# Performance work log

Measured on AMD Instinct MI355X. Metric: run time of the kernel, lower is better.

The kernel has to match this reference:

```python
import jax, jax.numpy as jnp
import numpy as np

N, A, B, H = 16, 2048, 2048, 64


def setup_inputs() -> dict:
    key = jax.random.key(0)
    k1, k2, k3, k4 = jax.random.split(key, 4)
    query = jax.random.normal(k1, (N, A, H), dtype=jnp.float32)
    key_t = jax.random.normal(k2, (N, B, H), dtype=jnp.float32)
    value = jax.random.normal(k3, (N, B, H), dtype=jnp.float32)
    mask = jax.random.randint(k4, (N, B), 0, 2).astype(bool)  # True = masked out
    return {"query": query, "key": key_t, "value": value, "mask": mask}


def reference(query, key, value, mask):
    # attention_product: scaled dot product -> (n, a, b) logits
    h = query.shape[-1]
    scale = 1.0 / jnp.sqrt(jnp.asarray(h, dtype=query.dtype))
    logit = jnp.einsum("nah,nbh->nab", query, key) * scale
    # mask (n, b) broadcast over query axis; masked positions -> -inf
    logit = jnp.where(mask[:, None, :], -jnp.inf, logit)
    attn = jax.nn.softmax(logit, axis=-1)
    # dropout_rate = 0.0 (eval) -> identity
    context = jnp.einsum("nab,nbh->nah", attn, value)
    return context
```

## Files before the change

kernel.cpp:

```cpp
#include <hip/hip_runtime.h>

#define NB 16
#define AQ 2048
#define BKV 2048
#define HD 64

#define QSCALE 0.18033688f
#define MBIAS -43000.0f
#define DTHR 8.0f

typedef float f32x4 __attribute__((ext_vector_type(4)));
typedef float f32x16 __attribute__((ext_vector_type(16)));
typedef short bf16x8 __attribute__((ext_vector_type(8)));
typedef int int4v __attribute__((ext_vector_type(4)));

__device__ __forceinline__ short f2bf(float f) {
  return __builtin_bit_cast(short, static_cast<__bf16>(f));
}
__device__ __forceinline__ unsigned pk2(float a, float b) {
  unsigned lo = (unsigned short)f2bf(a);
  unsigned hh = (unsigned short)f2bf(b);
  return lo | (hh << 16);
}

__global__ __launch_bounds__(256) void prepack(const float* __restrict__ K,
                                               const float* __restrict__ V,
                                               const int* __restrict__ M,
                                               short* __restrict__ Kb,
                                               short* __restrict__ Vt,
                                               unsigned* __restrict__ Mb) {
  if (blockIdx.x < 1024) {
    size_t base = ((size_t)blockIdx.x * 256 + threadIdx.x) * 8;
    f32x4 a = *(const f32x4*)(K + base);
    f32x4 b = *(const f32x4*)(K + base + 4);
    bf16x8 o;
#pragma unroll
    for (int i = 0; i < 4; ++i) {
      o[i] = f2bf(a[i]);
      o[i + 4] = f2bf(b[i]);
    }
    *(bf16x8*)(Kb + base) = o;
  } else if (blockIdx.x < 1536) {
    unsigned vb = blockIdx.x - 1024;
    int n = vb >> 5;
    int b0 = (vb & 31) * 64;
    int t = threadIdx.x;
    __shared__ short tile[64][68];
    int rb = t >> 4;
    int hc = (t & 15) * 4;
#pragma unroll
    for (int j = 0; j < 4; ++j) {
      int r = rb + 16 * j;
      f32x4 v = *(const f32x4*)(V + ((size_t)n * BKV + b0 + r) * HD + hc);
#pragma unroll
      for (int i = 0; i < 4; ++i) tile[r][hc + i] = f2bf(v[i]);
    }
    __syncthreads();
    int hr = t >> 2;
    int bb = (t & 3) * 16;
    bf16x8 o0, o1;
#pragma unroll
    for (int j = 0; j < 8; ++j) {
      o0[j] = tile[bb + j][hr];
      o1[j] = tile[bb + 8 + j][hr];
    }
    short* dst = Vt + ((size_t)n * HD + hr) * BKV + b0 + bb;
    *(bf16x8*)dst = o0;
    *(bf16x8*)(dst + 8) = o1;
  } else {
    unsigned gw = (blockIdx.x - 1536) * 256 + threadIdx.x;
    int n = (int)(gw >> 6);
    int ww = (int)(gw & 63u);
    const int* src = M + (size_t)n * BKV + ww * 32;
    unsigned bits = 0;
#pragma unroll
    for (int j = 0; j < 32; ++j) bits |= (src[j] ? 1u : 0u) << j;
    Mb[n * 64 + ww] = bits;
  }
}

template <int PRE>
__global__ __launch_bounds__(256, 3) void attn_fwd(
    const float* __restrict__ Q, const float* __restrict__ K,
    const float* __restrict__ V, const int* __restrict__ M,
    const short* __restrict__ Kb, const short* __restrict__ Vt,
    const unsigned* __restrict__ Mb, float* __restrict__ O) {
  unsigned orig = blockIdx.x;
  unsigned wg = (orig & 7u) * 128u + (orig >> 3);
  int n = (int)(wg >> 6);
  int q0 = (int)(wg & 63u) * 32;

  int w = threadIdx.x >> 6;
  int lane = threadIdx.x & 63;
  int hi = lane >> 5;
  int li = lane & 31;

  const float* Qn = Q + (size_t)n * AQ * HD;
  const float* Kn = K + (size_t)n * BKV * HD;
  const float* Vn = V + (size_t)n * BKV * HD;
  const short* Kbn = Kb + (size_t)n * BKV * HD;
  const short* Vtn = Vt + (size_t)n * HD * BKV;
  const unsigned* Mbn = Mb + (size_t)n * 64;
  const int* Mn = M + (size_t)n * BKV;

  __shared__ __align__(16) float pacc[4][32][68];
  __shared__ float Ml[4][2][32];

  bf16x8 qb[4];
#pragma unroll
  for (int ks = 0; ks < 4; ++ks) {
    const float* qp = Qn + (size_t)(q0 + li) * HD + 16 * ks + 8 * hi;
    f32x4 a = *(const f32x4*)qp;
    f32x4 b = *(const f32x4*)(qp + 4);
#pragma unroll
    for (int i = 0; i < 4; ++i) {
      qb[ks][i] = f2bf(a[i] * QSCALE);
      qb[ks][i + 4] = f2bf(b[i] * QSCALE);
    }
  }

  f32x16 acc0 = {};
  f32x16 acc1 = {};
  float m_run = -1e30f;
  float l_run = 0.f;

  const int bstart = w * (BKV / 4);

  auto LOADK = [&](int b0, bf16x8(&ka)[4]) {
#pragma unroll
    for (int ks = 0; ks < 4; ++ks) {
      if constexpr (PRE) {
        ka[ks] = *(const bf16x8*)(Kbn + (size_t)(b0 + li) * HD + 16 * ks + 8 * hi);
      } else {
        const float* kp = Kn + (size_t)(b0 + li) * HD + 16 * ks + 8 * hi;
        f32x4 k0 = *(const f32x4*)kp;
        f32x4 k1 = *(const f32x4*)(kp + 4);
#pragma unroll
        for (int i = 0; i < 4; ++i) {
          ka[ks][i] = f2bf(k0[i]);
          ka[ks][i + 4] = f2bf(k1[i]);
        }
      }
    }
  };
  auto LOADMB = [&](int b0) -> unsigned {
    if constexpr (PRE) return Mbn[b0 >> 5];
    return 0u;
  };

  auto TILE = [&](int b0, const bf16x8(&ka)[4], unsigned mb) {
    bf16x8 va0, va1, va2, va3;
    if constexpr (PRE) {
      const short* vp0 = Vtn + (size_t)li * BKV + b0 + 8 * hi;
      const short* vp1 = Vtn + (size_t)(32 + li) * BKV + b0 + 8 * hi;
      va0 = *(const bf16x8*)vp0;
      va1 = *(const bf16x8*)(vp0 + 16);
      va2 = *(const bf16x8*)vp1;
      va3 = *(const bf16x8*)(vp1 + 16);
    } else {
#pragma unroll
      for (int j = 0; j < 8; ++j) {
        va0[j] = f2bf(Vn[(size_t)(b0 + 8 * hi + j) * HD + li]);
        va1[j] = f2bf(Vn[(size_t)(b0 + 16 + 8 * hi + j) * HD + li]);
        va2[j] = f2bf(Vn[(size_t)(b0 + 8 * hi + j) * HD + 32 + li]);
        va3[j] = f2bf(Vn[(size_t)(b0 + 16 + 8 * hi + j) * HD + 32 + li]);
      }
    }

    f32x16 st;
    if constexpr (PRE) {
      unsigned ub = mb >> (4 * hi);
#pragma unroll
      for (int r = 0; r < 16; ++r) {
        int pos = (r & 3) + 8 * (r >> 2);
        st[r] = ((ub >> pos) & 1u) ? MBIAS : 0.f;
      }
    } else {
      int4v mv[4];
#pragma unroll
      for (int j = 0; j < 4; ++j) mv[j] = *(const int4v*)(Mn + b0 + 8 * j + 4 * hi);
#pragma unroll
      for (int j = 0; j < 4; ++j)
#pragma unroll
        for (int r = 0; r < 4; ++r) st[4 * j + r] = mv[j][r] ? MBIAS : 0.f;
    }

#pragma unroll
    for (int ks = 0; ks < 4; ++ks)
      st = __builtin_amdgcn_mfma_f32_32x32x16_bf16(ka[ks], qb[ks], st, 0, 0, 0);

    float a0 = fmaxf(fmaxf(st[0], st[1]), st[2]);
    float a1 = fmaxf(fmaxf(st[3], st[4]), st[5]);
    float a2 = fmaxf(fmaxf(st[6], st[7]), st[8]);
    float a3 = fmaxf(fmaxf(st[9], st[10]), st[11]);
    float a4 = fmaxf(fmaxf(st[12], st[13]), st[14]);
    float mt = fmaxf(fmaxf(fmaxf(a0, a1), fmaxf(a2, a3)), fmaxf(a4, st[15]));
    mt = fmaxf(mt, __shfl_xor(mt, 32));

    if (!__all(mt - m_run <= DTHR)) {
      float m_new = fmaxf(m_run, mt);
      float fac = exp2f(m_run - m_new);
      l_run *= fac;
#pragma unroll
      for (int i = 0; i < 16; ++i) {
        acc0[i] *= fac;
        acc1[i] *= fac;
      }
      m_run = m_new;
    }

#pragma unroll
    for (int i = 0; i < 16; ++i) st[i] = exp2f(st[i] - m_run);
    float s0 = (st[0] + st[1]) + (st[2] + st[3]);
    float s1 = (st[4] + st[5]) + (st[6] + st[7]);
    float s2 = (st[8] + st[9]) + (st[10] + st[11]);
    float s3 = (st[12] + st[13]) + (st[14] + st[15]);
    float rs = (s0 + s1) + (s2 + s3);
    rs += __shfl_xor(rs, 32);
    l_run += rs;

    unsigned w8[8];
#pragma unroll
    for (int j = 0; j < 8; ++j) w8[j] = pk2(st[2 * j], st[2 * j + 1]);
    auto s02 = __builtin_amdgcn_permlane32_swap((int)w8[0], (int)w8[2], false, false);
    auto s13 = __builtin_amdgcn_permlane32_swap((int)w8[1], (int)w8[3], false, false);
    auto s46 = __builtin_amdgcn_permlane32_swap((int)w8[4], (int)w8[6], false, false);
    auto s57 = __builtin_amdgcn_permlane32_swap((int)w8[5], (int)w8[7], false, false);
    int4v p0 = {static_cast<int>(s02[0]), static_cast<int>(s13[0]),
                static_cast<int>(s02[1]), static_cast<int>(s13[1])};
    int4v p1 = {static_cast<int>(s46[0]), static_cast<int>(s57[0]),
                static_cast<int>(s46[1]), static_cast<int>(s57[1])};
    bf16x8 pb0 = __builtin_bit_cast(bf16x8, p0);
    bf16x8 pb1 = __builtin_bit_cast(bf16x8, p1);

    acc0 = __builtin_amdgcn_mfma_f32_32x32x16_bf16(va0, pb0, acc0, 0, 0, 0);
    acc0 = __builtin_amdgcn_mfma_f32_32x32x16_bf16(va1, pb1, acc0, 0, 0, 0);
    acc1 = __builtin_amdgcn_mfma_f32_32x32x16_bf16(va2, pb0, acc1, 0, 0, 0);
    acc1 = __builtin_amdgcn_mfma_f32_32x32x16_bf16(va3, pb1, acc1, 0, 0, 0);
  };

  bf16x8 kaA[4], kaB[4];
  LOADK(bstart, kaA);
  unsigned mbA = LOADMB(bstart), mbB;
#pragma unroll 1
  for (int t = 0; t < 16; t += 2) {
    const int b0 = bstart + t * 32;
    LOADK(b0 + 32, kaB);
    mbB = LOADMB(b0 + 32);
    TILE(b0, kaA, mbA);
    if (t < 14) {
      LOADK(b0 + 64, kaA);
      mbA = LOADMB(b0 + 64);
    }
    TILE(b0 + 32, kaB, mbB);
  }

  if (hi == 0) {
    Ml[w][0][li] = m_run;
    Ml[w][1][li] = l_run;
  }
#pragma unroll
  for (int reg = 0; reg < 16; ++reg) {
    int hrow = (reg & 3) + 8 * (reg >> 2) + 4 * hi;
    pacc[w][li][hrow] = acc0[reg];
    pacc[w][li][32 + hrow] = acc1[reg];
  }
  __syncthreads();

  {
    int tid = threadIdx.x;
    int q = tid >> 3;
    int hb = (tid & 7) * 8;
    float m0 = Ml[0][0][q], m1 = Ml[1][0][q];
    float m2 = Ml[2][0][q], m3 = Ml[3][0][q];
    float mmax = fmaxf(fmaxf(m0, m1), fmaxf(m2, m3));
    float f[4] = {exp2f(m0 - mmax), exp2f(m1 - mmax), exp2f(m2 - mmax),
                  exp2f(m3 - mmax)};
    float l = f[0] * Ml[0][1][q] + f[1] * Ml[1][1][q] + f[2] * Ml[2][1][q] +
              f[3] * Ml[3][1][q];
    float inv = 1.0f / l;
    float* op = O + ((size_t)n * AQ + q0 + q) * HD + hb;
#pragma unroll
    for (int t = 0; t < 2; ++t) {
      f32x4 o = {0.f, 0.f, 0.f, 0.f};
#pragma unroll
      for (int ww = 0; ww < 4; ++ww) {
        f32x4 a = *(const f32x4*)&pacc[ww][q][hb + 4 * t];
#pragma unroll
        for (int i = 0; i < 4; ++i) o[i] += f[ww] * a[i];
      }
      f32x4 res;
#pragma unroll
      for (int i = 0; i < 4; ++i) res[i] = o[i] * inv;
      *(f32x4*)(op + 4 * t) = res;
    }
  }
}

extern "C" void kernel_launch(void* const* d_in, const int* in_sizes, int n_in,
                              void* d_out, int out_size, void* d_ws, size_t ws_size,
                              hipStream_t stream) {
  const float* q = (const float*)d_in[0];
  const float* k = (const float*)d_in[1];
  const float* v = (const float*)d_in[2];
  const int* m = (const int*)d_in[3];
  float* o = (float*)d_out;

  const size_t kv_elems = (size_t)NB * BKV * HD;
  const size_t mb_words = (size_t)NB * 64;
  const size_t need = kv_elems * 2 * sizeof(short) + mb_words * 4;

  if (ws_size >= need) {
    short* kb = (short*)d_ws;
    short* vt = kb + kv_elems;
    unsigned* mb = (unsigned*)(vt + kv_elems);
    prepack<<<dim3(1540), dim3(256), 0, stream>>>(k, v, m, kb, vt, mb);
    attn_fwd<1><<<dim3(NB * (AQ / 32)), dim3(256), 0, stream>>>(q, k, v, m, kb, vt, mb, o);
  } else {
    attn_fwd<0><<<dim3(NB * (AQ / 32)), dim3(256), 0, stream>>>(q, k, v, m, nullptr, nullptr, nullptr, o);
  }
}
```

Before: 140.9 us.

## Drop prepack kernel and convert K/V/mask to bf16 inline in attention

Removes the separate prepack kernel that converted K to bf16, transposed V to bf16 and bit-packed the mask into workspace. The attention kernel now always reads fp32 K, V and the int mask directly and converts them per tile. This saves a kernel launch and the extra write/read round trip through workspace. In exchange each block loads twice the bytes for K and V, uses strided scalar V loads, and repeats the conversion work across the 64 query blocks per batch.

```diff
diff --git a/kernel.cpp b/kernel.cpp
--- a/kernel.cpp
+++ b/kernel.cpp
@@ -23,68 +23,10 @@
   return lo | (hh << 16);
 }
 
-__global__ __launch_bounds__(256) void prepack(const float* __restrict__ K,
-                                               const float* __restrict__ V,
-                                               const int* __restrict__ M,
-                                               short* __restrict__ Kb,
-                                               short* __restrict__ Vt,
-                                               unsigned* __restrict__ Mb) {
-  if (blockIdx.x < 1024) {
-    size_t base = ((size_t)blockIdx.x * 256 + threadIdx.x) * 8;
-    f32x4 a = *(const f32x4*)(K + base);
-    f32x4 b = *(const f32x4*)(K + base + 4);
-    bf16x8 o;
-#pragma unroll
-    for (int i = 0; i < 4; ++i) {
-      o[i] = f2bf(a[i]);
-      o[i + 4] = f2bf(b[i]);
-    }
-    *(bf16x8*)(Kb + base) = o;
-  } else if (blockIdx.x < 1536) {
-    unsigned vb = blockIdx.x - 1024;
-    int n = vb >> 5;
-    int b0 = (vb & 31) * 64;
-    int t = threadIdx.x;
-    __shared__ short tile[64][68];
-    int rb = t >> 4;
-    int hc = (t & 15) * 4;
-#pragma unroll
-    for (int j = 0; j < 4; ++j) {
-      int r = rb + 16 * j;
-      f32x4 v = *(const f32x4*)(V + ((size_t)n * BKV + b0 + r) * HD + hc);
-#pragma unroll
-      for (int i = 0; i < 4; ++i) tile[r][hc + i] = f2bf(v[i]);
-    }
-    __syncthreads();
-    int hr = t >> 2;
-    int bb = (t & 3) * 16;
-    bf16x8 o0, o1;
-#pragma unroll
-    for (int j = 0; j < 8; ++j) {
-      o0[j] = tile[bb + j][hr];
-      o1[j] = tile[bb + 8 + j][hr];
-    }
-    short* dst = Vt + ((size_t)n * HD + hr) * BKV + b0 + bb;
-    *(bf16x8*)dst = o0;
-    *(bf16x8*)(dst + 8) = o1;
-  } else {
-    unsigned gw = (blockIdx.x - 1536) * 256 + threadIdx.x;
-    int n = (int)(gw >> 6);
-    int ww = (int)(gw & 63u);
-    const int* src = M + (size_t)n * BKV + ww * 32;
-    unsigned bits = 0;
-#pragma unroll
-    for (int j = 0; j < 32; ++j) bits |= (src[j] ? 1u : 0u) << j;
-    Mb[n * 64 + ww] = bits;
-  }
-}
-
-template <int PRE>
 __global__ __launch_bounds__(256, 3) void attn_fwd(
     const float* __restrict__ Q, const float* __restrict__ K,
     const float* __restrict__ V, const int* __restrict__ M,
-    const short* __restrict__ Kb, const short* __restrict__ Vt,
-    const unsigned* __restrict__ Mb, float* __restrict__ O) {
+    float* __restrict__ O) {
   unsigned orig = blockIdx.x;
   unsigned wg = (orig & 7u) * 128u + (orig >> 3);
   int n = (int)(wg >> 6);
@@ -98,9 +40,6 @@
   const float* Qn = Q + (size_t)n * AQ * HD;
   const float* Kn = K + (size_t)n * BKV * HD;
   const float* Vn = V + (size_t)n * BKV * HD;
-  const short* Kbn = Kb + (size_t)n * BKV * HD;
-  const short* Vtn = Vt + (size_t)n * HD * BKV;
-  const unsigned* Mbn = Mb + (size_t)n * 64;
   const int* Mn = M + (size_t)n * BKV;
 
   __shared__ __align__(16) float pacc[4][32][68];
@@ -129,61 +68,37 @@
   auto LOADK = [&](int b0, bf16x8(&ka)[4]) {
 #pragma unroll
     for (int ks = 0; ks < 4; ++ks) {
-      if constexpr (PRE) {
-        ka[ks] = *(const bf16x8*)(Kbn + (size_t)(b0 + li) * HD + 16 * ks + 8 * hi);
-      } else {
-        const float* kp = Kn + (size_t)(b0 + li) * HD + 16 * ks + 8 * hi;
-        f32x4 k0 = *(const f32x4*)kp;
-        f32x4 k1 = *(const f32x4*)(kp + 4);
-#pragma unroll
-        for (int i = 0; i < 4; ++i) {
-          ka[ks][i] = f2bf(k0[i]);
-          ka[ks][i + 4] = f2bf(k1[i]);
-        }
+      const float* kp = Kn + (size_t)(b0 + li) * HD + 16 * ks + 8 * hi;
+      f32x4 k0 = *(const f32x4*)kp;
+      f32x4 k1 = *(const f32x4*)(kp + 4);
+#pragma unroll
+      for (int i = 0; i < 4; ++i) {
+        ka[ks][i] = f2bf(k0[i]);
+        ka[ks][i + 4] = f2bf(k1[i]);
       }
     }
   };
-  auto LOADMB = [&](int b0) -> unsigned {
-    if constexpr (PRE) return Mbn[b0 >> 5];
-    return 0u;
-  };
-
-  auto TILE = [&](int b0, const bf16x8(&ka)[4], unsigned mb) {
+
+  auto TILE = [&](int b0, const bf16x8(&ka)[4]) {
     bf16x8 va0, va1, va2, va3;
-    if constexpr (PRE) {
-      const short* vp0 = Vtn + (size_t)li * BKV + b0 + 8 * hi;
-      const short* vp1 = Vtn + (size_t)(32 + li) * BKV + b0 + 8 * hi;
-      va0 = *(const bf16x8*)vp0;
-      va1 = *(const bf16x8*)(vp0 + 16);
-      va2 = *(const bf16x8*)vp1;
-      va3 = *(const bf16x8*)(vp1 + 16);
-    } else {
-#pragma unroll
-      for (int j = 0; j < 8; ++j) {
-        va0[j] = f2bf(Vn[(size_t)(b0 + 8 * hi + j) * HD + li]);
-        va1[j] = f2bf(Vn[(size_t)(b0 + 16 + 8 * hi + j) * HD + li]);
-        va2[j] = f2bf(Vn[(size_t)(b0 + 8 * hi + j) * HD + 32 + li]);
-        va3[j] = f2bf(Vn[(size_t)(b0 + 16 + 8 * hi + j) * HD + 32 + li]);
-      }
-    }
-
+#pragma unroll
+    for (int j = 0; j < 8; ++j) {
+      const float* vr0 = Vn + (size_t)(b0 + 8 * hi + j) * HD;
+      const float* vr1 = Vn + (size_t)(b0 + 16 + 8 * hi + j) * HD;
+      va0[j] = f2bf(vr0[li]);
+      va2[j] = f2bf(vr0[32 + li]);
+      va1[j] = f2bf(vr1[li]);
+      va3[j] = f2bf(vr1[32 + li]);
+    }
+
+    int4v mv[4];
+#pragma unroll
+    for (int j = 0; j < 4; ++j) mv[j] = *(const int4v*)(Mn + b0 + 8 * j + 4 * hi);
     f32x16 st;
-    if constexpr (PRE) {
-      unsigned ub = mb >> (4 * hi);
-#pragma unroll
-      for (int r = 0; r < 16; ++r) {
-        int pos = (r & 3) + 8 * (r >> 2);
-        st[r] = ((ub >> pos) & 1u) ? MBIAS : 0.f;
-      }
-    } else {
-      int4v mv[4];
-#pragma unroll
-      for (int j = 0; j < 4; ++j) mv[j] = *(const int4v*)(Mn + b0 + 8 * j + 4 * hi);
-#pragma unroll
-      for (int j = 0; j < 4; ++j)
-#pragma unroll
-        for (int r = 0; r < 4; ++r) st[4 * j + r] = mv[j][r] ? MBIAS : 0.f;
-    }
+#pragma unroll
+    for (int j = 0; j < 4; ++j)
+#pragma unroll
+      for (int r = 0; r < 4; ++r) st[4 * j + r] = mv[j][r] ? MBIAS : 0.f;
 
 #pragma unroll
     for (int ks = 0; ks < 4; ++ks)
@@ -241,18 +156,13 @@
 
   bf16x8 kaA[4], kaB[4];
   LOADK(bstart, kaA);
-  unsigned mbA = LOADMB(bstart), mbB;
 #pragma unroll 1
   for (int t = 0; t < 16; t += 2) {
     const int b0 = bstart + t * 32;
     LOADK(b0 + 32, kaB);
-    mbB = LOADMB(b0 + 32);
-    TILE(b0, kaA, mbA);
-    if (t < 14) {
-      LOADK(b0 + 64, kaA);
-      mbA = LOADMB(b0 + 64);
-    }
-    TILE(b0 + 32, kaB, mbB);
+    TILE(b0, kaA);
+    if (t < 14) LOADK(b0 + 64, kaA);
+    TILE(b0 + 32, kaB);
   }
 
   if (hi == 0) {
@@ -305,18 +215,5 @@
   const float* v = (const float*)d_in[2];
   const int* m = (const int*)d_in[3];
   float* o = (float*)d_out;
-
-  const size_t kv_elems = (size_t)NB * BKV * HD;
-  const size_t mb_words = (size_t)NB * 64;
-  const size_t need = kv_elems * 2 * sizeof(short) + mb_words * 4;
-
-  if (ws_size >= need) {
-    short* kb = (short*)d_ws;
-    short* vt = kb + kv_elems;
-    unsigned* mb = (unsigned*)(vt + kv_elems);
-    prepack<<<dim3(1540), dim3(256), 0, stream>>>(k, v, m, kb, vt, mb);
-    attn_fwd<1><<<dim3(NB * (AQ / 32)), dim3(256), 0, stream>>>(q, k, v, m, kb, vt, mb, o);
-  } else {
-    attn_fwd<0><<<dim3(NB * (AQ / 32)), dim3(256), 0, stream>>>(q, k, v, m, nullptr, nullptr, nullptr, o);
-  }
-}
+  attn_fwd<<<dim3(NB * (AQ / 32)), dim3(256), 0, stream>>>(q, k, v, m, o);
+}
```

New measurement: 161.1 us. 1.14x slower.

## Software-pipeline QK and softmax-PV stages across tiles, use permlane32 reductions

Applied to the files above, without the earlier changes.

Splits the per-tile body into QK, softmax+PV, and V-load stages and schedules the next tile's QK MFMAs before the current tile's softmax. The aim is to overlap matrix-core work with the exp/max ALU work and to prefetch V one tile ahead. Cross-half reductions now use permlane32_swap instead of __shfl_xor, which avoids LDS-based shuffles. The cost is more live registers (two score tiles plus K and V buffers), which may lower occupancy or cause spills.

```diff
diff --git a/kernel.cpp b/kernel.cpp
--- a/kernel.cpp
+++ b/kernel.cpp
@@ -21,6 +21,18 @@
   unsigned lo = (unsigned short)f2bf(a);
   unsigned hh = (unsigned short)f2bf(b);
   return lo | (hh << 16);
+}
+__device__ __forceinline__ float xmax32(float x) {
+  int xi = __builtin_bit_cast(int, x);
+  auto p = __builtin_amdgcn_permlane32_swap(xi, xi, false, false);
+  return fmaxf(__builtin_bit_cast(float, (int)p[0]),
+               __builtin_bit_cast(float, (int)p[1]));
+}
+__device__ __forceinline__ float xadd32(float x) {
+  int xi = __builtin_bit_cast(int, x);
+  auto p = __builtin_amdgcn_permlane32_swap(xi, xi, false, false);
+  return __builtin_bit_cast(float, (int)p[0]) +
+         __builtin_bit_cast(float, (int)p[1]);
 }
 
 __global__ __launch_bounds__(256) void prepack(const float* __restrict__ K,
@@ -147,9 +159,7 @@
     if constexpr (PRE) return Mbn[b0 >> 5];
     return 0u;
   };
-
-  auto TILE = [&](int b0, const bf16x8(&ka)[4], unsigned mb) {
-    bf16x8 va0, va1, va2, va3;
+  auto LOADV = [&](int b0, bf16x8& va0, bf16x8& va1, bf16x8& va2, bf16x8& va3) {
     if constexpr (PRE) {
       const short* vp0 = Vtn + (size_t)li * BKV + b0 + 8 * hi;
       const short* vp1 = Vtn + (size_t)(32 + li) * BKV + b0 + 8 * hi;
@@ -160,13 +170,17 @@
     } else {
 #pragma unroll
       for (int j = 0; j < 8; ++j) {
-        va0[j] = f2bf(Vn[(size_t)(b0 + 8 * hi + j) * HD + li]);
-        va1[j] = f2bf(Vn[(size_t)(b0 + 16 + 8 * hi + j) * HD + li]);
-        va2[j] = f2bf(Vn[(size_t)(b0 + 8 * hi + j) * HD + 32 + li]);
-        va3[j] = f2bf(Vn[(size_t)(b0 + 16 + 8 * hi + j) * HD + 32 + li]);
-      }
-    }
-
+        const float* vr0 = Vn + (size_t)(b0 + 8 * hi + j) * HD;
+        const float* vr1 = Vn + (size_t)(b0 + 16 + 8 * hi + j) * HD;
+        va0[j] = f2bf(vr0[li]);
+        va2[j] = f2bf(vr0[32 + li]);
+        va1[j] = f2bf(vr1[li]);
+        va3[j] = f2bf(vr1[32 + li]);
+      }
+    }
+  };
+
+  auto QK = [&](int b0, const bf16x8(&ka)[4], unsigned mb) -> f32x16 {
     f32x16 st;
     if constexpr (PRE) {
       unsigned ub = mb >> (4 * hi);
@@ -184,18 +198,21 @@
 #pragma unroll
         for (int r = 0; r < 4; ++r) st[4 * j + r] = mv[j][r] ? MBIAS : 0.f;
     }
-
 #pragma unroll
     for (int ks = 0; ks < 4; ++ks)
       st = __builtin_amdgcn_mfma_f32_32x32x16_bf16(ka[ks], qb[ks], st, 0, 0, 0);
-
+    return st;
+  };
+
+  auto SMPV = [&](f32x16& st, const bf16x8& va0, const bf16x8& va1,
+                  const bf16x8& va2, const bf16x8& va3) {
     float a0 = fmaxf(fmaxf(st[0], st[1]), st[2]);
     float a1 = fmaxf(fmaxf(st[3], st[4]), st[5]);
     float a2 = fmaxf(fmaxf(st[6], st[7]), st[8]);
     float a3 = fmaxf(fmaxf(st[9], st[10]), st[11]);
     float a4 = fmaxf(fmaxf(st[12], st[13]), st[14]);
     float mt = fmaxf(fmaxf(fmaxf(a0, a1), fmaxf(a2, a3)), fmaxf(a4, st[15]));
-    mt = fmaxf(mt, __shfl_xor(mt, 32));
+    mt = xmax32(mt);
 
     if (!__all(mt - m_run <= DTHR)) {
       float m_new = fmaxf(m_run, mt);
@@ -215,9 +232,7 @@
     float s1 = (st[4] + st[5]) + (st[6] + st[7]);
     float s2 = (st[8] + st[9]) + (st[10] + st[11]);
     float s3 = (st[12] + st[13]) + (st[14] + st[15]);
-    float rs = (s0 + s1) + (s2 + s3);
-    rs += __shfl_xor(rs, 32);
-    l_run += rs;
+    l_run += xadd32((s0 + s1) + (s2 + s3));
 
     unsigned w8[8];
 #pragma unroll
@@ -239,20 +254,33 @@
     acc1 = __builtin_amdgcn_mfma_f32_32x32x16_bf16(va3, pb1, acc1, 0, 0, 0);
   };
 
-  bf16x8 kaA[4], kaB[4];
-  LOADK(bstart, kaA);
-  unsigned mbA = LOADMB(bstart), mbB;
+  bf16x8 ka0[4], ka1[4];
+  bf16x8 va0, va1, va2, va3;
+  LOADK(bstart, ka0);
+  unsigned mb0 = LOADMB(bstart);
+  LOADK(bstart + 32, ka1);
+  unsigned mb1 = LOADMB(bstart + 32);
+  LOADV(bstart, va0, va1, va2, va3);
+  f32x16 stA = QK(bstart, ka0, mb0);
+  f32x16 stB;
+
 #pragma unroll 1
   for (int t = 0; t < 16; t += 2) {
     const int b0 = bstart + t * 32;
-    LOADK(b0 + 32, kaB);
-    mbB = LOADMB(b0 + 32);
-    TILE(b0, kaA, mbA);
-    if (t < 14) {
-      LOADK(b0 + 64, kaA);
-      mbA = LOADMB(b0 + 64);
-    }
-    TILE(b0 + 32, kaB, mbB);
+    if (t + 2 < 16) {
+      LOADK(b0 + 64, ka0);
+      mb0 = LOADMB(b0 + 64);
+    }
+    stB = QK(b0 + 32, ka1, mb1);
+    SMPV(stA, va0, va1, va2, va3);
+    LOADV(b0 + 32, va0, va1, va2, va3);
+    if (t + 3 < 16) {
+      LOADK(b0 + 96, ka1);
+      mb1 = LOADMB(b0 + 96);
+    }
+    if (t + 2 < 16) stA = QK(b0 + 64, ka0, mb0);
+    SMPV(stB, va0, va1, va2, va3);
+    if (t + 2 < 16) LOADV(b0 + 64, va0, va1, va2, va3);
   }
 
   if (hi == 0) {
```

New measurement: 141.1 us. Within noise of the previous version (+0.2%).
